# Kernel tuning notes

Measured on AMD Instinct MI355X. Metric: run time of the kernel, lower is better.

The kernel has to match this reference:

```python
import jax, jax.numpy as jnp
import numpy as np

B, S, F, D = 64, 129, 768, 4
MOM = 0.9
EPS = 1e-6


def setup_inputs() -> dict:
    key = jax.random.key(0)
    ks = jax.random.split(key, 8)
    x = jax.random.normal(ks[0], (B, S, F), dtype=jnp.float32)
    labels = jax.random.randint(ks[1], (B,), 0, 16, dtype=jnp.int32)
    domain = jax.random.randint(ks[2], (B,), 0, D, dtype=jnp.int32)
    lmda = jax.random.beta(ks[3], 0.1, 0.1, (B, 1, 1)).astype(jnp.float32)
    d_rand = jax.random.randint(ks[4], (B,), 1, D, dtype=jnp.int32)  # range(1, num_domains)
    mean_buf = (0.1 * jax.random.normal(ks[5], (D, F))).astype(jnp.float32)
    var_buf = jax.random.uniform(ks[6], (D, F), minval=0.5, maxval=1.5, dtype=jnp.float32)
    hg_noise = jax.random.normal(ks[7], (B, S, F), dtype=jnp.float32)
    return {"input": x, "lmda": lmda, "mean_buf": mean_buf, "var_buf": var_buf,
            "hg_noise": hg_noise, "labels": labels, "domain": domain, "d_rand": d_rand}


def reference(input, lmda, mean_buf, var_buf, hg_noise, labels, domain, d_rand):
    x = input  # [B,S,F]
    b, s, f = x.shape
    d = mean_buf.shape[0]

    # --- per-domain mean/var over dims [0,1] (unbiased), momentum buffer update ---
    tok = x.reshape(b * s, f)
    seg = jnp.repeat(domain, s)  # [B*S]
    cnt = jax.ops.segment_sum(jnp.ones((b * s,), x.dtype), seg, num_segments=d)  # tokens/domain
    s1 = jax.ops.segment_sum(tok, seg, num_segments=d)          # [D,F]
    s2 = jax.ops.segment_sum(tok * tok, seg, num_segments=d)    # [D,F]
    n = cnt[:, None]
    mu_d = s1 / jnp.maximum(n, 1.0)
    var_d = (s2 - n * mu_d * mu_d) / jnp.maximum(n - 1.0, 1.0)  # unbiased, matches torch.var
    present = (cnt > 0)[:, None]
    new_mean = jnp.where(present, MOM * mean_buf + (1.0 - MOM) * mu_d, mean_buf)
    new_var = jnp.where(present, MOM * var_buf + (1.0 - MOM) * var_d, var_buf)

    # --- instance renorm over token dim (unbiased var) + cross-domain restyle ---
    mu_i = x.mean(1, keepdims=True)
    v_i = x.var(1, keepdims=True, ddof=1)
    x_normed = (x - mu_i) * jax.lax.rsqrt(v_i + EPS)
    ds = (domain + d_rand) % d
    x_new = x_normed * jnp.sqrt(new_var[ds] + EPS)[:, None, :] + new_mean[ds][:, None, :]
    x_mix = lmda * x + (1.0 - lmda) * x_new

    # --- Gaussian hallucinated samples from own-domain stats ---
    hg = new_mean[domain][:, None, :] + jnp.sqrt(new_var[domain] + EPS)[:, None, :] * hg_noise

    # --- pairwise euclidean distance + hard example mining + soft-margin triplet loss ---
    xe = jnp.concatenate([x, x_mix, hg], axis=0).reshape(3 * b, s * f)  # [3B, S*F]
    ln = jnp.concatenate([labels, labels, -jnp.ones((b,), labels.dtype)])
    sq = jnp.sum(xe * xe, axis=1)
    d2 = sq[:, None] + sq[None, :] - 2.0 * (xe @ xe.T)
    dist = jnp.sqrt(jnp.clip(d2, 1e-12))
    pos = ln[:, None] == ln[None, :]
    big = jnp.asarray(1e30, dist.dtype)
    dist_ap = jnp.max(jnp.where(pos, dist, -big), axis=1)
    dist_an = jnp.min(jnp.where(pos, big, dist), axis=1)
    tri_hard_loss = jnp.mean(jax.nn.softplus(dist_ap - dist_an))  # SoftMarginLoss, y=1

    return x_mix, tri_hard_loss, new_mean, new_var
```

## Files before the change

### kernel.cpp

```cpp
#include <hip/hip_runtime.h>
#include <math.h>

#define B_ 64
#define S_ 129
#define F_ 768
#define N3 192
#define GSZ 36864
#define GRID_MAIN 252

#define WS_S1   0
#define WS_S2   49152
#define WS_SQ   98304
#define WS_PART 98560

#define OUT_LOSS 6340608
#define OUT_NM   6340609
#define OUT_NV   6343681

typedef unsigned int uint;
using short8v = __attribute__((ext_vector_type(8))) short;
using float4v = __attribute__((ext_vector_type(4))) float;

__device__ __forceinline__ uint pack2(float a, float b) {
    uint ua = __float_as_uint(a);
    uint ub = __float_as_uint(b);
    uint ha = (ua + 0x7FFFu + ((ua >> 16) & 1u)) >> 16;
    uint hb = (ub + 0x7FFFu + ((ub >> 16) & 1u)) & 0xFFFF0000u;
    return hb | ha;
}

__device__ __forceinline__ void bf16_store8(char* lds, int row, int g,
                                            float4 v0, float4 v1) {
    uint4 H;
    H.x = pack2(v0.x, v0.y);
    H.y = pack2(v0.z, v0.w);
    H.z = pack2(v1.x, v1.y);
    H.w = pack2(v1.z, v1.w);
    *(uint4*)(lds + row * 128 + ((g ^ (row & 7)) << 4)) = H;
}

__device__ __forceinline__ float4 fma4(float4 a, float4 x, float4 b) {
    float4 r;
    r.x = fmaf(a.x, x.x, b.x); r.y = fmaf(a.y, x.y, b.y);
    r.z = fmaf(a.z, x.z, b.z); r.w = fmaf(a.w, x.w, b.w);
    return r;
}

__global__ void k_stats(const float* __restrict__ x,
                        float* __restrict__ s1, float* __restrict__ s2,
                        float* __restrict__ sqw, float* __restrict__ out_loss) {
    __shared__ float4 r1[512], r2[512];
    if (blockIdx.x == 0) {
        if (threadIdx.x == 0) out_loss[0] = 0.0f;
        if (threadIdx.x < N3) sqw[threadIdx.x] = 0.0f;
    }
    int b = blockIdx.x / 3, fg = blockIdx.x % 3;
    int c = threadIdx.x & 63, sp = threadIdx.x >> 6;
    int f = fg * 256 + c * 4;
    const float* p = x + (size_t)b * S_ * F_ + f;
    int s0 = sp * 16;
    int se = s0 + 16 + (sp == 7 ? 1 : 0);
    float4 a1 = {0.f,0.f,0.f,0.f}, a2 = {0.f,0.f,0.f,0.f};
#pragma unroll 4
    for (int s = s0; s < se; ++s) {
        float4 v = *(const float4*)(p + s * F_);
        a1.x += v.x; a1.y += v.y; a1.z += v.z; a1.w += v.w;
        a2.x += v.x*v.x; a2.y += v.y*v.y; a2.z += v.z*v.z; a2.w += v.w*v.w;
    }
    r1[threadIdx.x] = a1; r2[threadIdx.x] = a2;
    __syncthreads();
    if (sp == 0) {
        float4 t1 = r1[c], t2 = r2[c];
#pragma unroll
        for (int k = 1; k < 8; ++k) {
            float4 u1 = r1[k * 64 + c], u2 = r2[k * 64 + c];
            t1.x += u1.x; t1.y += u1.y; t1.z += u1.z; t1.w += u1.w;
            t2.x += u2.x; t2.y += u2.y; t2.z += u2.z; t2.w += u2.w;
        }
        *(float4*)(s1 + b * F_ + f) = t1;
        *(float4*)(s2 + b * F_ + f) = t2;
    }
}

template <bool EXCL>
__global__ __launch_bounds__(512, 2)
void k_main(const float* __restrict__ x, const float* __restrict__ hgn,
            const float* __restrict__ s1, const float* __restrict__ s2,
            const float* __restrict__ mean_buf, const float* __restrict__ var_buf,
            const float* __restrict__ lmda, const int* __restrict__ domain,
            const int* __restrict__ d_rand,
            float* __restrict__ xmix, float* __restrict__ out_nm,
            float* __restrict__ out_nv,
            float* part, float* __restrict__ sqw, int npart) {
    __shared__ __align__(16) char LDS[49152];
    __shared__ float NMV[4][64];
    __shared__ float SVV[4][64];

    int tid = threadIdx.x;
    int bid = blockIdx.x;
    int fc = bid % 12, sb = bid / 12;
    int f0 = fc * 64;
    int b = tid >> 3, g = tid & 7;
    int w = tid >> 6;
    int wr = (w >> 2) * 96, wc = (w & 3) * 48;
    int lane = tid & 63, m = lane & 15, qd = lane >> 4;

    size_t gA = ((size_t)b * S_ + sb) * F_ + f0 + (g << 3);
    float4 XA0 = ((const float4*)(x + gA))[0];
    float4 XA1 = ((const float4*)(x + gA))[1];
    float4 NA0 = ((const float4*)(hgn + gA))[0];
    float4 NA1 = ((const float4*)(hgn + gA))[1];
    size_t gB = ((size_t)b * S_ + sb + 21) * F_ + f0 + (g << 3);
    float4 XB0 = ((const float4*)(x + gB))[0];
    float4 XB1 = ((const float4*)(x + gB))[1];
    float4 NB0 = ((const float4*)(hgn + gB))[0];
    float4 NB1 = ((const float4*)(hgn + gB))[1];

    if (tid < 256) {
        int d = tid & 3, fl = tid >> 2;
        int f = f0 + fl;
        float a1 = 0.f, a2 = 0.f, cnt = 0.f;
#pragma unroll 8
        for (int bb = 0; bb < B_; ++bb) {
            bool mk = (domain[bb] == d);
            a1  += mk ? s1[bb * F_ + f] : 0.f;
            a2  += mk ? s2[bb * F_ + f] : 0.f;
            cnt += mk ? 1.f : 0.f;
        }
        float nm, nv;
        if (cnt > 0.f) {
            float n = cnt * (float)S_;
            float mu = a1 / n;
            float var = (a2 - n * mu * mu) / fmaxf(n - 1.f, 1.f);
            nm = 0.9f * mean_buf[d * F_ + f] + 0.1f * mu;
            nv = 0.9f * var_buf[d * F_ + f] + 0.1f * var;
        } else {
            nm = mean_buf[d * F_ + f];
            nv = var_buf[d * F_ + f];
        }
        NMV[d][fl] = nm;
        SVV[d][fl] = sqrtf(nv + 1e-6f);
        if (sb == 0) { out_nm[d * F_ + f] = nm; out_nv[d * F_ + f] = nv; }
    }
    __syncthreads();

    int cb = b * F_ + f0 + (g << 3);
    float4 S1a = ((const float4*)(s1 + cb))[0], S1b = ((const float4*)(s1 + cb))[1];
    float4 S2a = ((const float4*)(s2 + cb))[0], S2b = ((const float4*)(s2 + cb))[1];
    int dm = domain[b];
    int dsd = (dm + d_rand[b]) & 3;
    float lam = lmda[b];
    float4 C1a, C1b, C0a, C0b, HMa, HMb, HSa, HSb;
#define COEF(SC1, SC2, FL, RC1, RC0, RHM, RHS) {            \
        float mu = (SC1) * (1.0f / (float)S_);              \
        float v  = ((SC2) - (float)S_ * mu * mu) * (1.0f / (float)(S_ - 1)); \
        float r  = rsqrtf(v + 1e-6f);                       \
        float sv = SVV[dsd][FL];                            \
        float rs = r * sv;                                  \
        RC1 = lam + (1.0f - lam) * rs;                      \
        RC0 = (1.0f - lam) * (NMV[dsd][FL] - mu * rs);      \
        RHM = NMV[dm][FL];                                  \
        RHS = SVV[dm][FL]; }
    {
        int fb = g << 3;
        COEF(S1a.x, S2a.x, fb + 0, C1a.x, C0a.x, HMa.x, HSa.x);
        COEF(S1a.y, S2a.y, fb + 1, C1a.y, C0a.y, HMa.y, HSa.y);
        COEF(S1a.z, S2a.z, fb + 2, C1a.z, C0a.z, HMa.z, HSa.z);
        COEF(S1a.w, S2a.w, fb + 3, C1a.w, C0a.w, HMa.w, HSa.w);
        COEF(S1b.x, S2b.x, fb + 4, C1b.x, C0b.x, HMb.x, HSb.x);
        COEF(S1b.y, S2b.y, fb + 5, C1b.y, C0b.y, HMb.y, HSb.y);
        COEF(S1b.z, S2b.z, fb + 6, C1b.z, C0b.z, HMb.z, HSb.z);
        COEF(S1b.w, S2b.w, fb + 7, C1b.w, C0b.w, HMb.w, HSb.w);
    }
#undef COEF

    float4v acc[6][3];
#pragma unroll
    for (int i = 0; i < 6; ++i)
#pragma unroll
        for (int j = 0; j < 3; ++j)
            acc[i][j] = (float4v){0.f, 0.f, 0.f, 0.f};

#define STAGE_CHUNK(PL, X0_, X1_, N0_, N1_, GOFF_)                           \
    {                                                                        \
        float4 M0 = fma4(C1a, X0_, C0a);                                     \
        float4 M1 = fma4(C1b, X1_, C0b);                                     \
        ((float4*)(xmix + GOFF_))[0] = M0;                                   \
        ((float4*)(xmix + GOFF_))[1] = M1;                                   \
        float4 H0 = fma4(HSa, N0_, HMa);                                     \
        float4 H1 = fma4(HSb, N1_, HMb);                                     \
        bf16_store8(LDS, (PL) * 192 + b, g, X0_, X1_);                       \
        bf16_store8(LDS, (PL) * 192 + 64 + b, g, M0, M1);                    \
        bf16_store8(LDS, (PL) * 192 + 128 + b, g, H0, H1);                   \
    }

#define MFMA_PLANE(PL)                                                       \
        _Pragma("unroll")                                                    \
        for (int t = 0; t < 2; ++t) {                                        \
            short8v A[6];                                                    \
            _Pragma("unroll")                                                \
            for (int i = 0; i < 6; ++i) {                                    \
                int row = wr + i * 16 + m;                                   \
                int go = (((t << 2) + qd) ^ (row & 7)) << 4;                 \
                A[i] = *(const short8v*)(LDS + ((PL) * 192 + row) * 128 + go); \
            }                                                                \
            _Pragma("unroll")                                                \
            for (int j = 0; j < 3; ++j) {                                    \
                int row = wc + j * 16 + m;                                   \
                int go = (((t << 2) + qd) ^ (row & 7)) << 4;                 \
                short8v Bv = *(const short8v*)(LDS + ((PL) * 192 + row) * 128 + go); \
                _Pragma("unroll")                                            \
                for (int i = 0; i < 6; ++i)                                  \
                    acc[i][j] = __builtin_amdgcn_mfma_f32_16x16x32_bf16(     \
                        A[i], Bv, acc[i][j], 0, 0, 0);                       \
            }                                                                \
        }

    for (int s = sb; s < S_; s += 42) {
        bool haveB = (s + 21 < S_);
        STAGE_CHUNK(0, XA0, XA1, NA0, NA1, gA);
        if (haveB) STAGE_CHUNK(1, XB0, XB1, NB0, NB1, gB);
        __syncthreads();

        if (s + 42 < S_) {
            gA = ((size_t)b * S_ + s + 42) * F_ + f0 + (g << 3);
            XA0 = ((const float4*)(x + gA))[0];
            XA1 = ((const float4*)(x + gA))[1];
            NA0 = ((const float4*)(hgn + gA))[0];
            NA1 = ((const float4*)(hgn + gA))[1];
        }
        if (s + 63 < S_) {
            gB = ((size_t)b * S_ + s + 63) * F_ + f0 + (g << 3);
            XB0 = ((const float4*)(x + gB))[0];
            XB1 = ((const float4*)(x + gB))[1];
            NB0 = ((const float4*)(hgn + gB))[0];
            NB1 = ((const float4*)(hgn + gB))[1];
        }

        MFMA_PLANE(0);
        if (haveB) MFMA_PLANE(1);
        __syncthreads();
    }
#undef STAGE_CHUNK
#undef MFMA_PLANE

    float* T = (float*)LDS;
    const int PADW = 196;
    float* dst = part + (size_t)(EXCL ? bid : (bid % npart)) * GSZ;
    int lrb = (wr ? 16 : 0) + (qd << 2);
    int lr2 = tid >> 4;
#pragma unroll
    for (int i = 0; i < 6; ++i) {
        __syncthreads();
#pragma unroll
        for (int j = 0; j < 3; ++j) {
            int colb = wc + j * 16 + m;
#pragma unroll
            for (int r = 0; r < 4; ++r)
                T[(lrb + r) * PADW + colb] = acc[i][j][r];
        }
        __syncthreads();
        int grow = i * 16 + (lr2 & 15) + (lr2 >> 4) * 96;
#pragma unroll
        for (int k = 0; k < 3; ++k) {
            int c4 = k * 16 + (tid & 15);
            float4 vv = *(const float4*)&T[lr2 * PADW + (c4 << 2)];
            int o = grow * N3 + (c4 << 2);
            if (EXCL) {
                *(float4*)(dst + o) = vv;
            } else {
                atomicAdd(dst + o + 0, vv.x);
                atomicAdd(dst + o + 1, vv.y);
                atomicAdd(dst + o + 2, vv.z);
                atomicAdd(dst + o + 3, vv.w);
            }
        }
        if (tid < 32) {
            int dr = i * 16 + (tid & 15) + (tid >> 4) * 96;
            atomicAdd(sqw + dr, T[tid * PADW + dr]);
        }
    }
}

__global__ void k_loss(const float* __restrict__ part, const float* __restrict__ sqw,
                       const int* __restrict__ labels,
                       float* __restrict__ out_loss, int npart) {
    __shared__ float ROW[2][N3];
    __shared__ float SQS[N3];
    __shared__ int   LN[N3];
    __shared__ float APW[3], ANW[3];
    int i = blockIdx.x, tid = threadIdx.x;
    if (tid < 384) {
        int c = tid % N3, h = tid / N3;
        float sacc = 0.f;
#pragma unroll 4
        for (int p = h; p < npart; p += 2)
            sacc += part[(size_t)p * GSZ + i * N3 + c];
        ROW[h][c] = sacc;
    }
    if (tid >= 320) {
        int c = tid - 320;
        SQS[c] = sqw[c];
        LN[c] = (c < 128) ? labels[c & 63] : -1;
    }
    __syncthreads();
    if (tid < N3) {
        float gij = ROW[0][tid] + ROW[1][tid];
        int li = LN[i];
        float d2 = SQS[i] + SQS[tid] - 2.0f * gij;
        float dist = sqrtf(fmaxf(d2, 1e-12f));
        bool pos = (li == LN[tid]);
        float ap = pos ? dist : -1e30f;
        float an = pos ? 1e30f : dist;
#pragma unroll
        for (int off = 32; off; off >>= 1) {
            ap = fmaxf(ap, __shfl_xor(ap, off));
            an = fminf(an, __shfl_xor(an, off));
        }
        if ((tid & 63) == 0) { APW[tid >> 6] = ap; ANW[tid >> 6] = an; }
    }
    __syncthreads();
    if (tid == 0) {
        float a = fmaxf(fmaxf(APW[0], APW[1]), APW[2]);
        float n = fminf(fminf(ANW[0], ANW[1]), ANW[2]);
        float xv = a - n;
        float sp = fmaxf(xv, 0.0f) + log1pf(expf(-fabsf(xv)));
        atomicAdd(out_loss, sp * (1.0f / (float)N3));
    }
}

extern "C" void kernel_launch(void* const* d_in, const int* in_sizes, int n_in,
                              void* d_out, int out_size, void* d_ws, size_t ws_size,
                              hipStream_t stream) {
    const float* x        = (const float*)d_in[0];
    const float* lmda     = (const float*)d_in[1];
    const float* mean_buf = (const float*)d_in[2];
    const float* var_buf  = (const float*)d_in[3];
    const float* hgn      = (const float*)d_in[4];
    const int*   labels   = (const int*)d_in[5];
    const int*   domain   = (const int*)d_in[6];
    const int*   d_rand   = (const int*)d_in[7];
    float* out = (float*)d_out;
    float* ws  = (float*)d_ws;

    long avail = (long)(ws_size / 4) - WS_PART;
    int npart = (int)(avail / GSZ);
    if (npart < 1) npart = 1;
    if (npart > GRID_MAIN) npart = GRID_MAIN;
    bool excl = (npart == GRID_MAIN);
    float* part = ws + WS_PART;
    float* sqw  = ws + WS_SQ;

    k_stats<<<dim3(192), dim3(512), 0, stream>>>(x, ws + WS_S1, ws + WS_S2,
                                                 sqw, out + OUT_LOSS);
    if (!excl) {
        hipMemsetAsync(part, 0, (size_t)npart * GSZ * 4, stream);
    }
    if (excl) {
        k_main<true><<<dim3(GRID_MAIN), dim3(512), 0, stream>>>(
            x, hgn, ws + WS_S1, ws + WS_S2, mean_buf, var_buf,
            lmda, domain, d_rand,
            out, out + OUT_NM, out + OUT_NV, part, sqw, npart);
    } else {
        k_main<false><<<dim3(GRID_MAIN), dim3(512), 0, stream>>>(
            x, hgn, ws + WS_S1, ws + WS_S2, mean_buf, var_buf,
            lmda, domain, d_rand,
            out, out + OUT_NM, out + OUT_NV, part, sqw, npart);
    }
    k_loss<<<dim3(N3), dim3(512), 0, stream>>>(part, sqw, labels,
                                               out + OUT_LOSS, npart);
}
```

Measured before the change: 141.3 us.

## Fuse loss reduction into main kernel via grid barrier and bf16 partial Gram slices

Merges the separate loss kernel into the main kernel. Each block now signals a global atomic counter, and the first 192 blocks spin until all blocks have arrived before reducing the per-block partial Gram slices. The partial Gram tiles are stored as packed bf16 instead of fp32, which halves partial-write and read-back traffic. The memset/atomic fallback path for small workspaces is also removed. This risks deadlock if the 252 blocks are not all co-resident. It also loses precision in the Gram sums, which feed a distance computed by cancellation. The counter is zeroed in k_stats, which keeps the spin barrier valid across calls.

```diff
diff --git a/kernel.cpp b/kernel.cpp
--- a/kernel.cpp
+++ b/kernel.cpp
@@ -5,8 +5,8 @@
 #define S_ 129
 #define F_ 768
 #define N3 192
-#define GSZ 36864
 #define GRID_MAIN 252
+#define PSLICE_U 18432
 
 #define WS_S1   0
 #define WS_S2   49152
@@ -52,7 +52,7 @@
     __shared__ float4 r1[512], r2[512];
     if (blockIdx.x == 0) {
         if (threadIdx.x == 0) out_loss[0] = 0.0f;
-        if (threadIdx.x < N3) sqw[threadIdx.x] = 0.0f;
+        if (threadIdx.x < 208) sqw[threadIdx.x] = 0.0f;
     }
     int b = blockIdx.x / 3, fg = blockIdx.x % 3;
     int c = threadIdx.x & 63, sp = threadIdx.x >> 6;
@@ -82,16 +82,15 @@
     }
 }
 
-template <bool EXCL>
 __global__ __launch_bounds__(512, 2)
-void k_main(const float* __restrict__ x, const float* __restrict__ hgn,
-            const float* __restrict__ s1, const float* __restrict__ s2,
-            const float* __restrict__ mean_buf, const float* __restrict__ var_buf,
-            const float* __restrict__ lmda, const int* __restrict__ domain,
-            const int* __restrict__ d_rand,
-            float* __restrict__ xmix, float* __restrict__ out_nm,
-            float* __restrict__ out_nv,
-            float* part, float* __restrict__ sqw, int npart) {
+void k_fused(const float* __restrict__ x, const float* __restrict__ hgn,
+             const float* __restrict__ s1, const float* __restrict__ s2,
+             const float* __restrict__ mean_buf, const float* __restrict__ var_buf,
+             const float* __restrict__ lmda, const int* __restrict__ domain,
+             const int* __restrict__ d_rand, const int* __restrict__ labels,
+             float* __restrict__ xmix, float* __restrict__ out_nm,
+             float* __restrict__ out_nv, float* __restrict__ out_loss,
+             uint* part_u, float* sqw) {
     __shared__ __align__(16) char LDS[49152];
     __shared__ float NMV[4][64];
     __shared__ float SVV[4][64];
@@ -246,7 +245,7 @@
 
     float* T = (float*)LDS;
     const int PADW = 196;
-    float* dst = part + (size_t)(EXCL ? bid : (bid % npart)) * GSZ;
+    uint* dst = part_u + (size_t)bid * PSLICE_U;
     int lrb = (wr ? 16 : 0) + (qd << 2);
     int lr2 = tid >> 4;
 #pragma unroll
@@ -265,67 +264,78 @@
         for (int k = 0; k < 3; ++k) {
             int c4 = k * 16 + (tid & 15);
             float4 vv = *(const float4*)&T[lr2 * PADW + (c4 << 2)];
-            int o = grow * N3 + (c4 << 2);
-            if (EXCL) {
-                *(float4*)(dst + o) = vv;
-            } else {
-                atomicAdd(dst + o + 0, vv.x);
-                atomicAdd(dst + o + 1, vv.y);
-                atomicAdd(dst + o + 2, vv.z);
-                atomicAdd(dst + o + 3, vv.w);
-            }
+            uint2 P;
+            P.x = pack2(vv.x, vv.y);
+            P.y = pack2(vv.z, vv.w);
+            *(uint2*)(dst + grow * 96 + (c4 << 1)) = P;
         }
         if (tid < 32) {
             int dr = i * 16 + (tid & 15) + (tid >> 4) * 96;
             atomicAdd(sqw + dr, T[tid * PADW + dr]);
         }
     }
-}
-
-__global__ void k_loss(const float* __restrict__ part, const float* __restrict__ sqw,
-                       const int* __restrict__ labels,
-                       float* __restrict__ out_loss, int npart) {
-    __shared__ float ROW[2][N3];
-    __shared__ float SQS[N3];
-    __shared__ int   LN[N3];
-    __shared__ float APW[3], ANW[3];
-    int i = blockIdx.x, tid = threadIdx.x;
-    if (tid < 384) {
-        int c = tid % N3, h = tid / N3;
-        float sacc = 0.f;
-#pragma unroll 4
-        for (int p = h; p < npart; p += 2)
-            sacc += part[(size_t)p * GSZ + i * N3 + c];
-        ROW[h][c] = sacc;
-    }
-    if (tid >= 320) {
-        int c = tid - 320;
-        SQS[c] = sqw[c];
-        LN[c] = (c < 128) ? labels[c & 63] : -1;
-    }
-    __syncthreads();
-    if (tid < N3) {
-        float gij = ROW[0][tid] + ROW[1][tid];
-        int li = LN[i];
-        float d2 = SQS[i] + SQS[tid] - 2.0f * gij;
-        float dist = sqrtf(fmaxf(d2, 1e-12f));
-        bool pos = (li == LN[tid]);
-        float ap = pos ? dist : -1e30f;
-        float an = pos ? 1e30f : dist;
-#pragma unroll
-        for (int off = 32; off; off >>= 1) {
-            ap = fmaxf(ap, __shfl_xor(ap, off));
-            an = fminf(an, __shfl_xor(an, off));
-        }
-        if ((tid & 63) == 0) { APW[tid >> 6] = ap; ANW[tid >> 6] = an; }
-    }
+
+    int* cnt = (int*)(sqw + 192);
+    __threadfence();
     __syncthreads();
     if (tid == 0) {
-        float a = fmaxf(fmaxf(APW[0], APW[1]), APW[2]);
-        float n = fminf(fminf(ANW[0], ANW[1]), ANW[2]);
-        float xv = a - n;
-        float sp = fmaxf(xv, 0.0f) + log1pf(expf(-fabsf(xv)));
-        atomicAdd(out_loss, sp * (1.0f / (float)N3));
+        atomicAdd(cnt, 1);
+        if (bid < N3) {
+            while (atomicAdd(cnt, 0) < GRID_MAIN) __builtin_amdgcn_s_sleep(8);
+        }
+    }
+    __syncthreads();
+    if (bid >= N3) return;
+    __threadfence();
+
+    {
+        float* ROWf = (float*)LDS;
+        float* SQS  = (float*)(LDS + 2048);
+        int*   LN   = (int*)(LDS + 2048 + 768);
+        float* APW  = (float*)(LDS + 4096);
+        float* ANW  = (float*)(LDS + 4096 + 16);
+        int i = bid;
+        if (tid < 384) {
+            int c = tid % N3, h = tid / N3;
+            int sh = (c & 1) << 4;
+            const uint* prow = part_u + (size_t)i * 96 + (c >> 1);
+            float sacc = 0.f;
+#pragma unroll 4
+            for (int p = h; p < GRID_MAIN; p += 2) {
+                uint u = prow[(size_t)p * PSLICE_U];
+                sacc += __uint_as_float(((u >> sh) & 0xFFFFu) << 16);
+            }
+            ROWf[h * N3 + c] = sacc;
+        }
+        if (tid >= 320) {
+            int c = tid - 320;
+            SQS[c] = sqw[c];
+            LN[c] = (c < 128) ? labels[c & 63] : -1;
+        }
+        __syncthreads();
+        if (tid < N3) {
+            float gij = ROWf[tid] + ROWf[N3 + tid];
+            int li = LN[i];
+            float d2 = SQS[i] + SQS[tid] - 2.0f * gij;
+            float dist = sqrtf(fmaxf(d2, 1e-12f));
+            bool pos = (li == LN[tid]);
+            float ap = pos ? dist : -1e30f;
+            float an = pos ? 1e30f : dist;
+#pragma unroll
+            for (int off = 32; off; off >>= 1) {
+                ap = fmaxf(ap, __shfl_xor(ap, off));
+                an = fminf(an, __shfl_xor(an, off));
+            }
+            if ((tid & 63) == 0) { APW[tid >> 6] = ap; ANW[tid >> 6] = an; }
+        }
+        __syncthreads();
+        if (tid == 0) {
+            float a = fmaxf(fmaxf(APW[0], APW[1]), APW[2]);
+            float n = fminf(fminf(ANW[0], ANW[1]), ANW[2]);
+            float xv = a - n;
+            float sp = fmaxf(xv, 0.0f) + log1pf(expf(-fabsf(xv)));
+            atomicAdd(out_loss, sp * (1.0f / (float)N3));
+        }
     }
 }
 
@@ -343,30 +353,14 @@
     float* out = (float*)d_out;
     float* ws  = (float*)d_ws;
 
-    long avail = (long)(ws_size / 4) - WS_PART;
-    int npart = (int)(avail / GSZ);
-    if (npart < 1) npart = 1;
-    if (npart > GRID_MAIN) npart = GRID_MAIN;
-    bool excl = (npart == GRID_MAIN);
-    float* part = ws + WS_PART;
     float* sqw  = ws + WS_SQ;
+    uint*  part = (uint*)(ws + WS_PART);
 
     k_stats<<<dim3(192), dim3(512), 0, stream>>>(x, ws + WS_S1, ws + WS_S2,
                                                  sqw, out + OUT_LOSS);
-    if (!excl) {
-        hipMemsetAsync(part, 0, (size_t)npart * GSZ * 4, stream);
-    }
-    if (excl) {
-        k_main<true><<<dim3(GRID_MAIN), dim3(512), 0, stream>>>(
-            x, hgn, ws + WS_S1, ws + WS_S2, mean_buf, var_buf,
-            lmda, domain, d_rand,
-            out, out + OUT_NM, out + OUT_NV, part, sqw, npart);
-    } else {
-        k_main<false><<<dim3(GRID_MAIN), dim3(512), 0, stream>>>(
-            x, hgn, ws + WS_S1, ws + WS_S2, mean_buf, var_buf,
-            lmda, domain, d_rand,
-            out, out + OUT_NM, out + OUT_NV, part, sqw, npart);
-    }
-    k_loss<<<dim3(N3), dim3(512), 0, stream>>>(part, sqw, labels,
-                                               out + OUT_LOSS, npart);
-}
+    k_fused<<<dim3(GRID_MAIN), dim3(512), 0, stream>>>(
+        x, hgn, ws + WS_S1, ws + WS_S2, mean_buf, var_buf,
+        lmda, domain, d_rand, labels,
+        out, out + OUT_NM, out + OUT_NV, out + OUT_LOSS,
+        part, sqw);
+}
```

New measurement: 225.5 us. 1.6x slower.
